# Performance work log

Measured on AMD Instinct MI355X. Metric: run time of the kernel, lower is better.

Reference implementation:

```python
import jax, jax.numpy as jnp
import numpy as np

B, N = 64, 1024            # graphs per batch, nodes per graph (batch = arange // N)
K_GRAPH, K_CONV = 95, 15   # knn_graph k, DynamicEdgeConv k
SLOPE = 0.01               # LeakyReLU default negative slope


def _lrelu(v):
    return jnp.where(v >= 0, v, SLOPE * v)


def _knn(feat, k, exclude_self):
    # feat: [B, N, F] -> within-graph neighbor indices [B, N, k]
    def one(p):
        sq = jnp.sum(p * p, axis=-1)
        d = sq[:, None] + sq[None, :] - 2.0 * (p @ p.T)  # [N, N] squared dists
        if exclude_self:
            d = d + jnp.eye(N, dtype=d.dtype) * 1e10
        return jax.lax.top_k(-d, k)[1]
    return jax.vmap(one)(feat)


def _gather(feat, idx):
    # feat [B,N,F], idx [B,N,k] -> [B,N,k,F]
    return jax.vmap(lambda f, i: f[i])(feat, idx)


def _edge_conv(feat, W1, b1, W2, b2):
    # DynamicEdgeConv: dynamic kNN on current features (self included, dist 0),
    # message = MLP([x_i, x_j - x_i]), aggregation = 'add'
    idx = _knn(feat, K_CONV, exclude_self=False)
    xj = _gather(feat, idx)                              # [B,N,k,F]
    xi = jnp.broadcast_to(feat[:, :, None, :], xj.shape)
    m = jnp.concatenate([xi, xj - xi], axis=-1)          # [B,N,k,2F]
    h = _lrelu(m @ W1 + b1)
    h = _lrelu(h @ W2 + b2)
    return jnp.sum(h, axis=2)                            # add-aggregate over neighbors


def setup_inputs() -> dict:
    key = jax.random.key(0)
    ks = jax.random.split(key, 24)

    def w(k, i, o):
        return (jax.random.normal(k, (i, o), jnp.float32) / np.sqrt(i)).astype(jnp.float32)

    def b(k, o):
        return (jax.random.normal(k, (o,), jnp.float32) * 0.01).astype(jnp.float32)

    return {
        "x": jax.random.normal(ks[0], (B * N, 1), jnp.float32),
        "pos": jax.random.normal(ks[1], (B * N, 3), jnp.float32),
        "tq": jax.random.normal(ks[2], (B * N, 1), jnp.float32),
        "batch": jnp.arange(B * N, dtype=jnp.int32) // N,
        "c1_W1": w(ks[3], 10, 64),  "c1_b1": b(ks[4], 64),
        "c1_W2": w(ks[5], 64, 64),  "c1_b2": b(ks[6], 64),
        "c2_W1": w(ks[7], 128, 128), "c2_b1": b(ks[8], 128),
        "c2_W2": w(ks[9], 128, 64),  "c2_b2": b(ks[10], 64),
        "l1_W1": w(ks[11], 197, 512), "l1_b1": b(ks[12], 512),
        "l1_W2": w(ks[13], 512, 256), "l1_b2": b(ks[14], 256),
        "m_W1": w(ks[15], 261, 256),  "m_b1": b(ks[16], 256),
        "m_W2": w(ks[17], 256, 3),    "m_b2": b(ks[18], 3),
    }


def reference(x, pos, tq, batch,
              c1_W1, c1_b1, c1_W2, c1_b2,
              c2_W1, c2_b1, c2_W2, c2_b2,
              l1_W1, l1_b1, l1_W2, l1_b2,
              m_W1, m_b1, m_W2, m_b2):
    xx = jnp.concatenate([tq, x, pos], axis=1)          # [B*N, 5]
    feat = xx.reshape(B, N, 5)

    # homophily (method='edge') per graph on knn_graph(k=95, no self-loops)
    idx95 = _knn(feat, K_GRAPH, exclude_self=True)      # [B,N,95]
    homo = []
    for c in range(5):
        y = feat[..., c]                                # [B,N]
        yj = _gather(y[..., None], idx95)[..., 0]       # [B,N,95]
        homo.append(jnp.mean((y[:, :, None] == yj).astype(feat.dtype), axis=(1, 2)))
    homo = jnp.stack(homo, axis=1)                      # [B,5]

    x1 = _edge_conv(feat, c1_W1, c1_b1, c1_W2, c1_b2)   # [B,N,64]
    x2 = _edge_conv(x1, c2_W1, c2_b1, c2_W2, c2_b2)     # [B,N,64]
    x3 = _edge_conv(x2, c2_W1, c2_b1, c2_W2, c2_b2)     # conv2 weights reused

    cat = jnp.concatenate([feat, x1, x2, x3], axis=-1)  # [B,N,197]
    out = _lrelu(cat @ l1_W1 + l1_b1) @ l1_W2 + l1_b2   # [B,N,256]

    # scatter_mean over batch (per-graph mean)
    nodes = out.reshape(B * N, 256)
    counts = jax.ops.segment_sum(jnp.ones((B * N,), nodes.dtype), batch, num_segments=B)
    d = jax.ops.segment_sum(nodes, batch, num_segments=B) / counts[:, None]  # [B,256]

    g = jnp.concatenate([d, homo], axis=1)              # [B,261]
    g = _lrelu(g)
    g = _lrelu(g @ m_W1 + m_b1)
    return g @ m_W2 + m_b2                              # [B,3]
```

## Files before the change

### kernel.cpp

```cpp
#include <hip/hip_runtime.h>

#define DEV __device__ __forceinline__

static constexpr int NB = 64;
static constexpr int NN = 1024;
static constexpr int NT = NB * NN;

DEV float lrelu(float v){ return v >= 0.f ? v : 0.01f * v; }

DEV unsigned keyf(float d){
  unsigned u = __float_as_uint(d);
  return (u & 0x80000000u) ? ~u : (u | 0x80000000u);
}

DEV void wave_lds_fence(){
  __builtin_amdgcn_wave_barrier();
  asm volatile("s_waitcnt lgkmcnt(0)" ::: "memory");
  __builtin_amdgcn_sched_barrier(0);
  __builtin_amdgcn_wave_barrier();
}

DEV void radix_kth(const unsigned long long* keys, int k, unsigned* hist,
                   unsigned long long& prefix_out, int& shift_out){
  int lane = threadIdx.x & 63;
  unsigned long long prefix = 0;
  unsigned kk = (unsigned)k;
  #pragma unroll 1
  for (int p = 0; p < 8; ++p){
    int shift = 56 - 8 * p;
    #pragma unroll
    for (int i = 0; i < 4; ++i) hist[lane * 4 + i] = 0u;
    wave_lds_fence();
    #pragma unroll
    for (int s = 0; s < 16; ++s){
      unsigned long long key = keys[s];
      bool match = (p == 0) || ((key >> (shift + 8)) == prefix);
      if (match) atomicAdd(&hist[(unsigned)(key >> shift) & 255u], 1u);
    }
    wave_lds_fence();
    unsigned c0 = hist[lane*4+0], c1 = hist[lane*4+1], c2 = hist[lane*4+2], c3 = hist[lane*4+3];
    unsigned s4 = c0 + c1 + c2 + c3;
    unsigned incl = s4;
    #pragma unroll
    for (int d = 1; d < 64; d <<= 1){
      unsigned t = (unsigned)__shfl_up((int)incl, d);
      if (lane >= d) incl += t;
    }
    unsigned excl = incl - s4;
    bool flag = (excl < kk) && (kk <= excl + s4);
    int bstar = 0; unsigned less = 0, cnt = 0;
    if (flag){
      unsigned cs[4] = {c0, c1, c2, c3};
      unsigned cum = excl;
      #pragma unroll
      for (int i = 0; i < 4; ++i){
        if (cnt == 0u && kk > cum && kk <= cum + cs[i]){
          bstar = lane * 4 + i; less = cum; cnt = cs[i];
        }
        cum += cs[i];
      }
    }
    unsigned long long bm = __ballot(flag);
    int src = __ffsll((long long)bm) - 1;
    bstar = __shfl(bstar, src);
    less  = (unsigned)__shfl((int)less, src);
    cnt   = (unsigned)__shfl((int)cnt, src);
    prefix = (prefix << 8) | (unsigned long long)(unsigned)bstar;
    kk -= less;
    if (kk == cnt){ prefix_out = prefix; shift_out = shift; return; }
  }
  prefix_out = prefix; shift_out = 0;
}

__global__ __launch_bounds__(256) void prep_kernel(
    const float* __restrict__ x, const float* __restrict__ pos, const float* __restrict__ tq,
    float* __restrict__ feat, float* __restrict__ sqv, unsigned* __restrict__ homoc){
  int n = blockIdx.x * 256 + threadIdx.x;
  if (n < NT){
    float f0 = tq[n], f1 = x[n], f2 = pos[n*3+0], f3 = pos[n*3+1], f4 = pos[n*3+2];
    feat[n*5+0] = f0; feat[n*5+1] = f1; feat[n*5+2] = f2; feat[n*5+3] = f3; feat[n*5+4] = f4;
    sqv[n] = f0*f0 + f1*f1 + f2*f2 + f3*f3 + f4*f4;
  }
  if (blockIdx.x == 0){
    for (int e = threadIdx.x; e < 320; e += 256) homoc[e] = 0u;
  }
}

__global__ __launch_bounds__(256) void knn5f_kernel(
    const float* __restrict__ feat, const float* __restrict__ sqv,
    int* __restrict__ idx_out, unsigned* __restrict__ homoc){
  __shared__ float fs[NN * 5];
  __shared__ float ss[NN];
  __shared__ unsigned hist[4][256];
  __shared__ unsigned wctr[4];
  int b = blockIdx.x >> 8;
  int q0 = (blockIdx.x & 255) * 4;
  const float* fg = feat + (size_t)b * NN * 5;
  for (int e = threadIdx.x; e < NN * 5; e += 256) fs[e] = fg[e];
  const float* sg = sqv + (size_t)b * NN;
  for (int e = threadIdx.x; e < NN; e += 256) ss[e] = sg[e];
  __syncthreads();
  int w = threadIdx.x >> 6, lane = threadIdx.x & 63;
  int q = q0 + w;
  float qf[5];
  #pragma unroll
  for (int c = 0; c < 5; ++c) qf[c] = fs[q*5+c];
  float sqq = ss[q];
  unsigned long long keys[16];
  #pragma unroll
  for (int s = 0; s < 16; ++s){
    int c = s * 64 + lane;
    float dot = qf[0]*fs[c*5+0] + qf[1]*fs[c*5+1] + qf[2]*fs[c*5+2] + qf[3]*fs[c*5+3] + qf[4]*fs[c*5+4];
    float d = sqq + ss[c] - 2.f * dot;
    keys[s] = ((unsigned long long)keyf(d) << 32) | (unsigned)c;
  }
  unsigned long long pfx; int sh;
  radix_kth(keys, 15, &hist[w][0], pfx, sh);
  if (lane == 0) wctr[w] = 0u;
  wave_lds_fence();
  #pragma unroll
  for (int s = 0; s < 16; ++s){
    unsigned long long key = keys[s];
    if ((key >> sh) <= pfx){
      unsigned pos = atomicAdd(&wctr[w], 1u);
      idx_out[(size_t)(b*NN + q) * 15 + pos] = b*NN + (int)(key & 0xffffffffull);
    }
  }
  #pragma unroll
  for (int s = 0; s < 16; ++s)
    if ((unsigned)(keys[s] & 0xffffffffull) == (unsigned)q) keys[s] = ~0ull;
  radix_kth(keys, 95, &hist[w][0], pfx, sh);
  unsigned cnt5[5] = {0,0,0,0,0};
  #pragma unroll
  for (int s = 0; s < 16; ++s){
    unsigned long long key = keys[s];
    if ((key >> sh) <= pfx){
      int c = (int)(key & 0xffffffffull);
      #pragma unroll
      for (int ch = 0; ch < 5; ++ch) cnt5[ch] += (fs[c*5+ch] == qf[ch]) ? 1u : 0u;
    }
  }
  #pragma unroll
  for (int ch = 0; ch < 5; ++ch){
    unsigned v = cnt5[ch];
    #pragma unroll
    for (int d = 32; d >= 1; d >>= 1) v += (unsigned)__shfl_xor((int)v, d);
    if (lane == 0) atomicAdd(&homoc[b*5+ch], v);
  }
}

__global__ __launch_bounds__(256) void knn64_kernel(
    const float* __restrict__ X, const float* __restrict__ sqv, int* __restrict__ idx_out){
  __shared__ __align__(16) float chunk[128 * 64];
  __shared__ float sqc[128];
  __shared__ __align__(16) float qf[4][64];
  __shared__ unsigned hist[4][256];
  __shared__ unsigned wctr[4];
  int b = blockIdx.x >> 8;
  int q0 = (blockIdx.x & 255) * 4;
  int w = threadIdx.x >> 6, lane = threadIdx.x & 63;
  int q = q0 + w;
  int qg = b * NN + q;
  qf[w][lane] = X[(size_t)qg * 64 + lane];
  float sqq = sqv[qg];
  float dist[16];
  #pragma unroll 1
  for (int ch = 0; ch < 8; ++ch){
    __syncthreads();
    {
      const float* xg = X + (size_t)(b * NN + ch * 128) * 64;
      #pragma unroll
      for (int r = 0; r < 8; ++r){
        int e = threadIdx.x + 256 * r;
        int c = e >> 4, f4 = e & 15;
        float4 v = *(const float4*)(xg + c * 64 + f4 * 4);
        *(float4*)&chunk[c * 64 + (((f4 ^ (c & 15))) << 2)] = v;
      }
      if (threadIdx.x < 128) sqc[threadIdx.x] = sqv[b * NN + ch * 128 + threadIdx.x];
    }
    __syncthreads();
    #pragma unroll
    for (int i = 0; i < 2; ++i){
      int cl = lane + 64 * i;
      float acc = 0.f;
      #pragma unroll
      for (int f4 = 0; f4 < 16; ++f4){
        float4 qv = *(const float4*)&qf[w][f4 * 4];
        float4 xv = *(const float4*)&chunk[cl * 64 + (((f4 ^ (cl & 15))) << 2)];
        acc += qv.x*xv.x + qv.y*xv.y + qv.z*xv.z + qv.w*xv.w;
      }
      dist[ch * 2 + i] = sqq + sqc[cl] - 2.f * acc;
    }
  }
  unsigned long long keys[16];
  #pragma unroll
  for (int s = 0; s < 16; ++s){
    int ch = s >> 1, i = s & 1;
    int c = ch * 128 + i * 64 + lane;
    keys[s] = ((unsigned long long)keyf(dist[s]) << 32) | (unsigned)c;
  }
  unsigned long long pfx; int sh;
  radix_kth(keys, 15, &hist[w][0], pfx, sh);
  if (lane == 0) wctr[w] = 0u;
  wave_lds_fence();
  #pragma unroll
  for (int s = 0; s < 16; ++s){
    unsigned long long key = keys[s];
    if ((key >> sh) <= pfx){
      unsigned pos = atomicAdd(&wctr[w], 1u);
      idx_out[(size_t)qg * 15 + pos] = b * NN + (int)(key & 0xffffffffull);
    }
  }
}

template<int F, int H1, int YS>
__global__ __launch_bounds__(256) void uv_kernel(
    const float* __restrict__ X, const float* __restrict__ W1, const float* __restrict__ b1,
    float* __restrict__ U, float* __restrict__ V){
  constexpr int HH = H1 / YS;
  __shared__ float w1s[2 * F * HH];
  constexpr int NPI = 256 / HH;
  __shared__ float xs[NPI][F];
  constexpr int NPB = 32;
  int node0 = blockIdx.x * NPB;
  int y0 = blockIdx.y * HH;
  for (int e = threadIdx.x; e < 2 * F * HH; e += 256)
    w1s[e] = W1[(size_t)(e / HH) * H1 + y0 + (e % HH)];
  int ol = threadIdx.x % HH, nn = threadIdx.x / HH;
  float b1o = b1[y0 + ol];
  for (int it = 0; it < NPB / NPI; ++it){
    __syncthreads();
    int nbase = node0 + it * NPI;
    for (int e = threadIdx.x; e < NPI * F; e += 256)
      xs[e / F][e % F] = X[(size_t)(nbase + e / F) * F + (e % F)];
    __syncthreads();
    float u = b1o, v = 0.f;
    #pragma unroll
    for (int f = 0; f < F; ++f){
      float xf = xs[nn][f];
      float wt = w1s[f * HH + ol], wb = w1s[(F + f) * HH + ol];
      u += xf * (wt - wb);
      v += xf * wb;
    }
    size_t node = nbase + nn;
    U[node * H1 + y0 + ol] = u;
    V[node * H1 + y0 + ol] = v;
  }
}

template<int H1, bool WRSQ>
__global__ __launch_bounds__(256) void edge_kernel(
    const float* __restrict__ U, const float* __restrict__ V,
    const int* __restrict__ idx15, const float* __restrict__ W2,
    const float* __restrict__ b2, float* __restrict__ out,
    float* __restrict__ sqv, int base){
  constexpr int H14 = H1 / 4;
  __shared__ __align__(16) float w2t[64 * H1];
  __shared__ __align__(16) float h1s[4][15 * H1];
  __shared__ int idxs[4][16];
  int w = threadIdx.x >> 6, lane = threadIdx.x & 63;
  int node_l = blockIdx.x * 4 + w;
  int node_g = base + node_l;
  for (int e = threadIdx.x; e < 64 * H14; e += 256){
    int o = e & 63, h4 = e >> 6;
    float vv[4];
    #pragma unroll
    for (int j = 0; j < 4; ++j) vv[j] = W2[(size_t)(h4 * 4 + j) * 64 + o];
    float* dst = &w2t[o * H1 + (((h4 ^ (o & 7))) << 2)];
    #pragma unroll
    for (int j = 0; j < 4; ++j) dst[j] = vv[j];
  }
  if (lane < 15) idxs[w][lane] = idx15[(size_t)node_g * 15 + lane] - base;
  __syncthreads();
  for (int e = lane; e < 15 * H14; e += 64){
    int j = e / H14, h4 = e % H14;
    int jn = idxs[w][j];
    float4 uu = *(const float4*)(U + (size_t)node_l * H1 + h4 * 4);
    float4 vv = *(const float4*)(V + (size_t)jn * H1 + h4 * 4);
    float4 h;
    h.x = lrelu(uu.x + vv.x); h.y = lrelu(uu.y + vv.y);
    h.z = lrelu(uu.z + vv.z); h.w = lrelu(uu.w + vv.w);
    *(float4*)&h1s[w][j * H1 + h4 * 4] = h;
  }
  __syncthreads();
  int o = lane;
  float acc[15];
  #pragma unroll
  for (int j = 0; j < 15; ++j) acc[j] = 0.f;
  for (int h4 = 0; h4 < H14; ++h4){
    float4 wv = *(const float4*)&w2t[o * H1 + (((h4 ^ (o & 7))) << 2)];
    #pragma unroll
    for (int j = 0; j < 15; ++j){
      float4 hv = *(const float4*)&h1s[w][j * H1 + h4 * 4];
      acc[j] += wv.x*hv.x + wv.y*hv.y + wv.z*hv.z + wv.w*hv.w;
    }
  }
  float b2o = b2[o];
  float s = 0.f;
  #pragma unroll
  for (int j = 0; j < 15; ++j) s += lrelu(acc[j] + b2o);
  out[(size_t)node_g * 64 + o] = s;
  if (WRSQ){
    float s2 = s * s;
    #pragma unroll
    for (int d = 1; d < 64; d <<= 1) s2 += __shfl_xor(s2, d);
    if (lane == 0) sqv[node_g] = s2;
  }
}

__global__ __launch_bounds__(256) void gemm1_kernel(
    const float* __restrict__ feat, const float* __restrict__ x1,
    const float* __restrict__ x2, const float* __restrict__ x3,
    const float* __restrict__ W1, const float* __restrict__ b1,
    float* __restrict__ hbuf, int base){
  __shared__ __align__(16) float As[16][64];
  __shared__ __align__(16) float Bs[16][64];
  int node0 = blockIdx.x * 64, n0 = blockIdx.y * 64;
  int tid = threadIdx.x, tx = tid & 15, ty = tid >> 4;
  float acc[4][4] = {};
  for (int k0 = 0; k0 < 197; k0 += 16){
    __syncthreads();
    #pragma unroll
    for (int r = 0; r < 4; ++r){
      int e = tid + 256 * r;
      int k = e >> 6, m = e & 63;
      int kk = k0 + k;
      size_t node = (size_t)base + node0 + m;
      float v;
      if (kk < 5) v = feat[node * 5 + kk];
      else if (kk < 69)  v = x1[node * 64 + kk - 5];
      else if (kk < 133) v = x2[node * 64 + kk - 69];
      else if (kk < 197) v = x3[node * 64 + kk - 133];
      else v = 0.f;
      As[k][m] = v;
      Bs[k][m] = (kk < 197) ? W1[(size_t)kk * 512 + n0 + m] : 0.f;
    }
    __syncthreads();
    #pragma unroll
    for (int k = 0; k < 16; ++k){
      float4 a = *(const float4*)&As[k][ty * 4];
      float4 bq = *(const float4*)&Bs[k][tx * 4];
      acc[0][0]+=a.x*bq.x; acc[0][1]+=a.x*bq.y; acc[0][2]+=a.x*bq.z; acc[0][3]+=a.x*bq.w;
      acc[1][0]+=a.y*bq.x; acc[1][1]+=a.y*bq.y; acc[1][2]+=a.y*bq.z; acc[1][3]+=a.y*bq.w;
      acc[2][0]+=a.z*bq.x; acc[2][1]+=a.z*bq.y; acc[2][2]+=a.z*bq.z; acc[2][3]+=a.z*bq.w;
      acc[3][0]+=a.w*bq.x; acc[3][1]+=a.w*bq.y; acc[3][2]+=a.w*bq.z; acc[3][3]+=a.w*bq.w;
    }
  }
  #pragma unroll
  for (int i = 0; i < 4; ++i){
    size_t node = node0 + ty * 4 + i;
    float4 st;
    st.x = lrelu(acc[i][0] + b1[n0 + tx*4 + 0]);
    st.y = lrelu(acc[i][1] + b1[n0 + tx*4 + 1]);
    st.z = lrelu(acc[i][2] + b1[n0 + tx*4 + 2]);
    st.w = lrelu(acc[i][3] + b1[n0 + tx*4 + 3]);
    *(float4*)(hbuf + node * 512 + n0 + tx * 4) = st;
  }
}

__global__ __launch_bounds__(256) void gemm2_kernel(
    const float* __restrict__ hbuf, const float* __restrict__ W2,
    const float* __restrict__ b2, float* __restrict__ parts, int base){
  __shared__ __align__(16) float As[16][64];
  __shared__ __align__(16) float Bs[16][64];
  __shared__ float red[16][64];
  int node0 = blockIdx.x * 64, n0 = blockIdx.y * 64;
  int tid = threadIdx.x, tx = tid & 15, ty = tid >> 4;
  float acc[4][4] = {};
  for (int k0 = 0; k0 < 512; k0 += 16){
    __syncthreads();
    {
      int m = tid >> 2, k4 = (tid & 3) * 4;
      float4 hv = *(const float4*)(hbuf + (size_t)(node0 + m) * 512 + k0 + k4);
      As[k4 + 0][m] = hv.x;
      As[k4 + 1][m] = hv.y;
      As[k4 + 2][m] = hv.z;
      As[k4 + 3][m] = hv.w;
      #pragma unroll
      for (int r = 0; r < 4; ++r){
        int e = tid + 256 * r;
        int k = e >> 6, n = e & 63;
        Bs[k][n] = W2[(size_t)(k0 + k) * 256 + n0 + n];
      }
    }
    __syncthreads();
    #pragma unroll
    for (int k = 0; k < 16; ++k){
      float4 a = *(const float4*)&As[k][ty * 4];
      float4 bq = *(const float4*)&Bs[k][tx * 4];
      acc[0][0]+=a.x*bq.x; acc[0][1]+=a.x*bq.y; acc[0][2]+=a.x*bq.z; acc[0][3]+=a.x*bq.w;
      acc[1][0]+=a.y*bq.x; acc[1][1]+=a.y*bq.y; acc[1][2]+=a.y*bq.z; acc[1][3]+=a.y*bq.w;
      acc[2][0]+=a.z*bq.x; acc[2][1]+=a.z*bq.y; acc[2][2]+=a.z*bq.z; acc[2][3]+=a.z*bq.w;
      acc[3][0]+=a.w*bq.x; acc[3][1]+=a.w*bq.y; acc[3][2]+=a.w*bq.z; acc[3][3]+=a.w*bq.w;
    }
  }
  float cs[4];
  #pragma unroll
  for (int c = 0; c < 4; ++c){
    float bb = b2[n0 + tx * 4 + c];
    cs[c] = (acc[0][c] + bb) + (acc[1][c] + bb) + (acc[2][c] + bb) + (acc[3][c] + bb);
  }
  __syncthreads();
  red[ty][tx*4+0] = cs[0]; red[ty][tx*4+1] = cs[1];
  red[ty][tx*4+2] = cs[2]; red[ty][tx*4+3] = cs[3];
  __syncthreads();
  if (tid < 64){
    float s = 0.f;
    #pragma unroll
    for (int t = 0; t < 16; ++t) s += red[t][tid];
    int node_g0 = base + node0;
    int g = node_g0 >> 10;
    int blk = (node_g0 >> 6) & 15;
    parts[(size_t)(g * 16 + blk) * 256 + n0 + tid] = s;
  }
}

__global__ __launch_bounds__(256) void final_kernel(
    const float* __restrict__ parts, const unsigned* __restrict__ homoc,
    const float* __restrict__ mW1, const float* __restrict__ mb1,
    const float* __restrict__ mW2, const float* __restrict__ mb2,
    float* __restrict__ out){
  __shared__ float gv[261];
  __shared__ float z[256];
  int g = blockIdx.x, t = threadIdx.x;
  float s = 0.f;
  #pragma unroll
  for (int p = 0; p < 16; ++p) s += parts[(size_t)(g * 16 + p) * 256 + t];
  float dmean = s * (1.f / 1024.f);
  gv[t] = lrelu(dmean);
  if (t < 5) gv[256 + t] = lrelu((float)homoc[g * 5 + t] * (1.f / 97280.f));
  __syncthreads();
  float acc = mb1[t];
  for (int f = 0; f < 261; ++f) acc += gv[f] * mW1[(size_t)f * 256 + t];
  z[t] = lrelu(acc);
  __syncthreads();
  if (t < 3){
    float o = mb2[t];
    for (int f = 0; f < 256; ++f) o += z[f] * mW2[f * 3 + t];
    out[g * 3 + t] = o;
  }
}

__global__ __launch_bounds__(64) void diag_kernel(float* out, float hostcode){
  if (threadIdx.x == 0 && hostcode != 0.f) out[0] = hostcode;
}

extern "C" void kernel_launch(void* const* d_in, const int* in_sizes, int n_in,
                              void* d_out, int out_size, void* d_ws, size_t ws_size,
                              hipStream_t stream){
  (void)out_size;
  static const int E[20] = {65536,196608,65536,65536,640,64,4096,64,16384,128,8192,64,
                            100864,512,131072,256,66816,256,768,3};
  int map[20];
  float hostcode = 0.f;
  bool runnable = true;
  for (int i = 0; i < 20; ++i) map[i] = (i < n_in) ? i : 0;
  if (n_in < 19){
    hostcode = 4.0e7f; runnable = false;
  } else {
    bool ident = (n_in >= 20);
    if (ident) for (int i = 0; i < 20; ++i) if (in_sizes[i] != E[i]) { ident = false; break; }
    if (!ident){
      bool drop = true;
      for (int i = 0; i < 19 && drop; ++i){
        int ei = (i < 3) ? i : i + 1;
        if (in_sizes[i] != E[ei]) drop = false;
      }
      bool tail = false;
      if (!drop && n_in >= 20){
        tail = true;
        for (int i = 0; i < 19 && tail; ++i){
          int ei = (i < 3) ? i : i + 1;
          if (in_sizes[i] != E[ei]) tail = false;
        }
        if (tail && in_sizes[19] != E[3]) tail = false;
      }
      if (drop){
        for (int i = 0; i < 3; ++i) map[i] = i;
        map[3] = 0;
        for (int i = 4; i < 20; ++i) map[i] = i - 1;
      } else if (tail){
        for (int i = 0; i < 3; ++i) map[i] = i;
        map[3] = 19;
        for (int i = 4; i < 20; ++i) map[i] = i - 1;
      } else {
        int firstbad = 0;
        for (int i = 0; i < 20; ++i){
          if (i >= n_in || in_sizes[i] != E[i]) { firstbad = i; break; }
        }
        hostcode = 2.0e7f + 1.0e6f * (float)firstbad;
      }
    }
  }
  const float* x    = (const float*)d_in[map[0]];
  const float* pos  = (const float*)d_in[map[1]];
  const float* tq   = (const float*)d_in[map[2]];
  const float* c1W1 = (const float*)d_in[map[4]];
  const float* c1b1 = (const float*)d_in[map[5]];
  const float* c1W2 = (const float*)d_in[map[6]];
  const float* c1b2 = (const float*)d_in[map[7]];
  const float* c2W1 = (const float*)d_in[map[8]];
  const float* c2b1 = (const float*)d_in[map[9]];
  const float* c2W2 = (const float*)d_in[map[10]];
  const float* c2b2 = (const float*)d_in[map[11]];
  const float* l1W1 = (const float*)d_in[map[12]];
  const float* l1b1 = (const float*)d_in[map[13]];
  const float* l1W2 = (const float*)d_in[map[14]];
  const float* l1b2 = (const float*)d_in[map[15]];
  const float* mW1  = (const float*)d_in[map[16]];
  const float* mb1  = (const float*)d_in[map[17]];
  const float* mW2  = (const float*)d_in[map[18]];
  const float* mb2  = (const float*)d_in[map[19]];

  char* wsb = (char*)d_ws;
  size_t off = 0;
  auto alloc = [&](size_t bytes) -> char* {
    char* p = wsb + off;
    off += (bytes + 255) & ~(size_t)255;
    return p;
  };
  float* feat  = (float*)alloc((size_t)NT * 5 * 4);
  float* sqv   = (float*)alloc((size_t)NT * 4);
  float* xf1   = (float*)alloc((size_t)NT * 64 * 4);
  float* xf2   = (float*)alloc((size_t)NT * 64 * 4);
  float* xf3   = (float*)alloc((size_t)NT * 64 * 4);
  int*   idx15 = (int*)alloc((size_t)NT * 15 * 4);
  unsigned* homoc = (unsigned*)alloc(320 * 4);
  float* parts = (float*)alloc((size_t)NB * 16 * 256 * 4);

  size_t fixed_off = off;
  int C = 4;
  while (C < 64 && fixed_off + (size_t)(NT / C) * 2048 + 256 > ws_size) C <<= 1;
  int chunkN = NT / C;
  bool wsbad = fixed_off + (size_t)chunkN * 2048 + 256 > ws_size;
  float* R    = (float*)alloc((size_t)chunkN * 2048);
  float* U    = R;
  float* V64  = R + (size_t)chunkN * 64;
  float* V128 = R + (size_t)chunkN * 128;
  float* hbuf = R;
  if (wsbad && hostcode == 0.f) hostcode = 5.0e6f;

  int ftype = 0;
  (void)hipGetLastError();
  #define LCK(ty) do { if (hipGetLastError() != hipSuccess && ftype == 0) ftype = (ty); } while(0)

  dim3 blk(256);
  if (runnable){
    prep_kernel<<<dim3((NT + 255) / 256), blk, 0, stream>>>(x, pos, tq, feat, sqv, homoc);
    LCK(1);
    knn5f_kernel<<<dim3(NB * 256), blk, 0, stream>>>(feat, sqv, idx15, homoc);
    LCK(2);

    if (!wsbad){
      for (int c = 0; c < C; ++c){
        int base = c * chunkN;
        uv_kernel<5, 64, 1><<<dim3(chunkN / 32, 1), blk, 0, stream>>>(feat + (size_t)base * 5, c1W1, c1b1, U, V64);
        LCK(4);
        edge_kernel<64, true><<<dim3(chunkN / 4), blk, 0, stream>>>(U, V64, idx15, c1W2, c1b2, xf1, sqv, base);
        LCK(5);
      }
      knn64_kernel<<<dim3(NB * 256), blk, 0, stream>>>(xf1, sqv, idx15);
      LCK(7);
      for (int c = 0; c < C; ++c){
        int base = c * chunkN;
        uv_kernel<64, 128, 2><<<dim3(chunkN / 32, 2), blk, 0, stream>>>(xf1 + (size_t)base * 64, c2W1, c2b1, U, V128);
        LCK(8);
        edge_kernel<128, true><<<dim3(chunkN / 4), blk, 0, stream>>>(U, V128, idx15, c2W2, c2b2, xf2, sqv, base);
        LCK(9);
      }
      knn64_kernel<<<dim3(NB * 256), blk, 0, stream>>>(xf2, sqv, idx15);
      LCK(7);
      for (int c = 0; c < C; ++c){
        int base = c * chunkN;
        uv_kernel<64, 128, 2><<<dim3(chunkN / 32, 2), blk, 0, stream>>>(xf2 + (size_t)base * 64, c2W1, c2b1, U, V128);
        LCK(8);
        edge_kernel<128, false><<<dim3(chunkN / 4), blk, 0, stream>>>(U, V128, idx15, c2W2, c2b2, xf3, sqv, base);
        LCK(9);
      }
      for (int c = 0; c < C; ++c){
        int base = c * chunkN;
        gemm1_kernel<<<dim3(chunkN / 64, 8), blk, 0, stream>>>(feat, xf1, xf2, xf3, l1W1, l1b1, hbuf, base);
        LCK(10);
        gemm2_kernel<<<dim3(chunkN / 64, 4), blk, 0, stream>>>(hbuf, l1W2, l1b2, parts, base);
        LCK(11);
      }
    }
    final_kernel<<<dim3(NB), blk, 0, stream>>>(parts, homoc, mW1, mb1, mW2, mb2, (float*)d_out);
    LCK(12);
  }
  if (ftype != 0 && hostcode == 0.f) hostcode = 1.0e7f * (float)ftype;
  diag_kernel<<<dim3(1), dim3(64), 0, stream>>>((float*)d_out, hostcode);
  #undef LCK
}
```

Baseline: 4.288 ms.

## Replace LDS histogram radix select with bitwise register radix select via popcount

Swaps the 8-bit-digit LDS-histogram top-k selection for a bit-by-bit radix select. Each lane packs one key bit per slot into a 16-bit mask, and counts are reduced across the wave with popcount and xor shuffles. Ties are broken by slot and lane bits instead of a packed 64-bit key, which removes the LDS atomics and histogram memory. The cost is up to 32+ wave reductions per selection instead of about 8 histogram passes, with an early exit once the selection is resolved.

```diff
diff --git a/kernel.cpp b/kernel.cpp
--- a/kernel.cpp
+++ b/kernel.cpp
@@ -20,56 +20,49 @@
   __builtin_amdgcn_wave_barrier();
 }
 
-DEV void radix_kth(const unsigned long long* keys, int k, unsigned* hist,
-                   unsigned long long& prefix_out, int& shift_out){
-  int lane = threadIdx.x & 63;
-  unsigned long long prefix = 0;
-  unsigned kk = (unsigned)k;
+DEV unsigned wavesum_u(unsigned v){
+  #pragma unroll
+  for (int d = 1; d < 64; d <<= 1) v += (unsigned)__shfl_xor((int)v, d);
+  return v;
+}
+
+DEV unsigned radix_sel(const unsigned* dk, int k, int lane){
+  unsigned active = 0xFFFFu, sel = 0u;
+  unsigned kk = (unsigned)k, ta = 1024u;
   #pragma unroll 1
-  for (int p = 0; p < 8; ++p){
-    int shift = 56 - 8 * p;
-    #pragma unroll
-    for (int i = 0; i < 4; ++i) hist[lane * 4 + i] = 0u;
-    wave_lds_fence();
-    #pragma unroll
-    for (int s = 0; s < 16; ++s){
-      unsigned long long key = keys[s];
-      bool match = (p == 0) || ((key >> (shift + 8)) == prefix);
-      if (match) atomicAdd(&hist[(unsigned)(key >> shift) & 255u], 1u);
-    }
-    wave_lds_fence();
-    unsigned c0 = hist[lane*4+0], c1 = hist[lane*4+1], c2 = hist[lane*4+2], c3 = hist[lane*4+3];
-    unsigned s4 = c0 + c1 + c2 + c3;
-    unsigned incl = s4;
-    #pragma unroll
-    for (int d = 1; d < 64; d <<= 1){
-      unsigned t = (unsigned)__shfl_up((int)incl, d);
-      if (lane >= d) incl += t;
-    }
-    unsigned excl = incl - s4;
-    bool flag = (excl < kk) && (kk <= excl + s4);
-    int bstar = 0; unsigned less = 0, cnt = 0;
-    if (flag){
-      unsigned cs[4] = {c0, c1, c2, c3};
-      unsigned cum = excl;
-      #pragma unroll
-      for (int i = 0; i < 4; ++i){
-        if (cnt == 0u && kk > cum && kk <= cum + cs[i]){
-          bstar = lane * 4 + i; less = cum; cnt = cs[i];
-        }
-        cum += cs[i];
-      }
-    }
-    unsigned long long bm = __ballot(flag);
-    int src = __ffsll((long long)bm) - 1;
-    bstar = __shfl(bstar, src);
-    less  = (unsigned)__shfl((int)less, src);
-    cnt   = (unsigned)__shfl((int)cnt, src);
-    prefix = (prefix << 8) | (unsigned long long)(unsigned)bstar;
-    kk -= less;
-    if (kk == cnt){ prefix_out = prefix; shift_out = shift; return; }
-  }
-  prefix_out = prefix; shift_out = 0;
+  for (int b = 31; b >= 0; --b){
+    unsigned m1 = 0u;
+    #pragma unroll
+    for (int s = 0; s < 16; ++s) m1 |= ((dk[s] >> b) & 1u) << s;
+    unsigned m0 = active & ~m1;
+    unsigned c0 = wavesum_u((unsigned)__popc(m0));
+    if (c0 >= kk){ active = m0; ta = c0; }
+    else { sel |= m0; kk -= c0; active &= m1; ta -= c0; }
+    if (ta == kk){ sel |= active; active = 0u; ta = 0u; }
+    if (__builtin_amdgcn_readfirstlane(ta) == 0u) return sel;
+  }
+  {
+    const unsigned smask[4] = {0xFF00u, 0xF0F0u, 0xCCCCu, 0xAAAAu};
+    #pragma unroll
+    for (int i = 0; i < 4; ++i){
+      unsigned m1 = smask[i];
+      unsigned m0 = active & ~m1;
+      unsigned c0 = wavesum_u((unsigned)__popc(m0));
+      if (c0 >= kk){ active = m0; ta = c0; }
+      else { sel |= m0; kk -= c0; active &= m1; ta -= c0; }
+      if (ta == kk){ sel |= active; active = 0u; ta = 0u; }
+    }
+    #pragma unroll
+    for (int b = 5; b >= 0; --b){
+      unsigned m1 = ((lane >> b) & 1) ? 0xFFFFu : 0u;
+      unsigned m0 = active & ~m1;
+      unsigned c0 = wavesum_u((unsigned)__popc(m0));
+      if (c0 >= kk){ active = m0; ta = c0; }
+      else { sel |= m0; kk -= c0; active &= m1; ta -= c0; }
+      if (ta == kk){ sel |= active; active = 0u; ta = 0u; }
+    }
+  }
+  return sel;
 }
 
 __global__ __launch_bounds__(256) void prep_kernel(
@@ -91,7 +84,6 @@
     int* __restrict__ idx_out, unsigned* __restrict__ homoc){
   __shared__ float fs[NN * 5];
   __shared__ float ss[NN];
-  __shared__ unsigned hist[4][256];
   __shared__ unsigned wctr[4];
   int b = blockIdx.x >> 8;
   int q0 = (blockIdx.x & 255) * 4;
@@ -106,36 +98,34 @@
   #pragma unroll
   for (int c = 0; c < 5; ++c) qf[c] = fs[q*5+c];
   float sqq = ss[q];
-  unsigned long long keys[16];
+  unsigned dk[16];
   #pragma unroll
   for (int s = 0; s < 16; ++s){
     int c = s * 64 + lane;
     float dot = qf[0]*fs[c*5+0] + qf[1]*fs[c*5+1] + qf[2]*fs[c*5+2] + qf[3]*fs[c*5+3] + qf[4]*fs[c*5+4];
     float d = sqq + ss[c] - 2.f * dot;
-    keys[s] = ((unsigned long long)keyf(d) << 32) | (unsigned)c;
-  }
-  unsigned long long pfx; int sh;
-  radix_kth(keys, 15, &hist[w][0], pfx, sh);
+    dk[s] = keyf(d);
+  }
+  unsigned sel = radix_sel(dk, 15, lane);
   if (lane == 0) wctr[w] = 0u;
   wave_lds_fence();
   #pragma unroll
   for (int s = 0; s < 16; ++s){
-    unsigned long long key = keys[s];
-    if ((key >> sh) <= pfx){
+    if ((sel >> s) & 1u){
       unsigned pos = atomicAdd(&wctr[w], 1u);
-      idx_out[(size_t)(b*NN + q) * 15 + pos] = b*NN + (int)(key & 0xffffffffull);
-    }
-  }
+      idx_out[(size_t)(b*NN + q) * 15 + pos] = b*NN + s*64 + lane;
+    }
+  }
+  int sq_s = q >> 6, sq_l = q & 63;
   #pragma unroll
   for (int s = 0; s < 16; ++s)
-    if ((unsigned)(keys[s] & 0xffffffffull) == (unsigned)q) keys[s] = ~0ull;
-  radix_kth(keys, 95, &hist[w][0], pfx, sh);
+    if (s == sq_s && lane == sq_l) dk[s] = 0xFFFFFFFFu;
+  unsigned sel2 = radix_sel(dk, 95, lane);
   unsigned cnt5[5] = {0,0,0,0,0};
   #pragma unroll
   for (int s = 0; s < 16; ++s){
-    unsigned long long key = keys[s];
-    if ((key >> sh) <= pfx){
-      int c = (int)(key & 0xffffffffull);
+    if ((sel2 >> s) & 1u){
+      int c = s * 64 + lane;
       #pragma unroll
       for (int ch = 0; ch < 5; ++ch) cnt5[ch] += (fs[c*5+ch] == qf[ch]) ? 1u : 0u;
     }
@@ -154,7 +144,6 @@
   __shared__ __align__(16) float chunk[128 * 64];
   __shared__ float sqc[128];
   __shared__ __align__(16) float qf[4][64];
-  __shared__ unsigned hist[4][256];
   __shared__ unsigned wctr[4];
   int b = blockIdx.x >> 8;
   int q0 = (blockIdx.x & 255) * 4;
@@ -192,23 +181,17 @@
       dist[ch * 2 + i] = sqq + sqc[cl] - 2.f * acc;
     }
   }
-  unsigned long long keys[16];
-  #pragma unroll
-  for (int s = 0; s < 16; ++s){
-    int ch = s >> 1, i = s & 1;
-    int c = ch * 128 + i * 64 + lane;
-    keys[s] = ((unsigned long long)keyf(dist[s]) << 32) | (unsigned)c;
-  }
-  unsigned long long pfx; int sh;
-  radix_kth(keys, 15, &hist[w][0], pfx, sh);
+  unsigned dk[16];
+  #pragma unroll
+  for (int s = 0; s < 16; ++s) dk[s] = keyf(dist[s]);
+  unsigned sel = radix_sel(dk, 15, lane);
   if (lane == 0) wctr[w] = 0u;
   wave_lds_fence();
   #pragma unroll
   for (int s = 0; s < 16; ++s){
-    unsigned long long key = keys[s];
-    if ((key >> sh) <= pfx){
+    if ((sel >> s) & 1u){
       unsigned pos = atomicAdd(&wctr[w], 1u);
-      idx_out[(size_t)qg * 15 + pos] = b * NN + (int)(key & 0xffffffffull);
+      idx_out[(size_t)qg * 15 + pos] = b * NN + s*64 + lane;
     }
   }
 }
```

New measurement: 3.981 ms. 7.2% less time.
